# Kernel tuning notes

Measured on AMD Instinct MI355X. Metric: run time of the kernel, lower is better.

Reference implementation:

```python
import jax, jax.numpy as jnp
import numpy as np

D = 1024
H = 8
B, S = 4, 2048


def setup_inputs() -> dict:
    key = jax.random.key(0)
    ks = jax.random.split(key, 11)
    s = 0.02
    return {
        "Q": jax.random.normal(ks[0], (B, S, D), jnp.float32),
        "K": jax.random.normal(ks[1], (B, S, D), jnp.float32),
        "V": jax.random.normal(ks[2], (B, S, D), jnp.float32),
        "WQ": jax.random.normal(ks[3], (D, D), jnp.float32) * s,
        "bQ": jax.random.normal(ks[4], (D,), jnp.float32) * s,
        "WK": jax.random.normal(ks[5], (D, D), jnp.float32) * s,
        "bK": jax.random.normal(ks[6], (D,), jnp.float32) * s,
        "WV": jax.random.normal(ks[7], (D, D), jnp.float32) * s,
        "bV": jax.random.normal(ks[8], (D,), jnp.float32) * s,
        "Wl": jax.random.normal(ks[9], (D, D * H), jnp.float32) * s,
        "bl": jax.random.normal(ks[10], (D,), jnp.float32) * s,
    }


def reference(Q, K, V, WQ, bQ, WK, bK, WV, bV, Wl, bl):
    # SelfAttention (weights shared across all heads in the original module)
    q = Q @ WQ.T + bQ  # [B,S,D]
    k = K @ WK.T + bK
    v = V @ WV.T + bV
    scale = 1.0 / np.sqrt(D).astype(np.float32)
    scores = jnp.einsum('bqd,bkd->bqk', q, k) * scale  # [B,S,S]
    attn = jax.nn.softmax(scores, axis=-1)
    Z = jnp.einsum('bqk,bkd->bqd', attn, v)  # [B,S,D]
    # concat of H identical copies, then linear(D*H -> D)
    Zcat = jnp.tile(Z, (1, 1, H))  # [B,S,D*H]
    return Zcat @ Wl.T + bl
```

## Files before the change

kernel.cpp:

```cpp
#include <hip/hip_runtime.h>
#include <stdint.h>

#define DEV __device__ __forceinline__

typedef __attribute__((ext_vector_type(8))) unsigned short frag8;
typedef __attribute__((ext_vector_type(4))) float f32x4;
typedef __attribute__((ext_vector_type(8))) unsigned short ushort8;
typedef __attribute__((ext_vector_type(4))) unsigned short ushort4v;

DEV unsigned short f2bf(float f) {
  union { float f; unsigned u; } x; x.f = f;
  unsigned r = x.u + 0x7fffu + ((x.u >> 16) & 1u);
  return (unsigned short)(r >> 16);
}
DEV float bf2f(unsigned short b) {
  union { unsigned u; float f; } x; x.u = ((unsigned)b) << 16;
  return x.f;
}

DEV void gload_lds16(const void* g, void* l) {
  __builtin_amdgcn_global_load_lds((const __attribute__((address_space(1))) void*)g,
                                   (__attribute__((address_space(3))) void*)l, 16, 0, 0);
}

DEV void mfma_bf16(f32x4& c, frag8 a, frag8 b) {
  asm("v_mfma_f32_16x16x32_bf16 %0, %1, %2, %0" : "+v"(c) : "v"(a), "v"(b));
}

DEV void wait_vm0_barrier() {
  asm volatile("s_waitcnt vmcnt(0)" ::: "memory");
  __builtin_amdgcn_s_barrier();
  asm volatile("" ::: "memory");
  __builtin_amdgcn_sched_barrier(0);
}

template<int BIAS, int SCALEF, int MODE>
__global__ __launch_bounds__(256)
void gemm_bt(const unsigned short* __restrict__ A,
             const unsigned short* __restrict__ Bm,
             const float* __restrict__ bias0, const float* __restrict__ bias1,
             const float* __restrict__ bias2,
             void* __restrict__ Cv,
             int N, int K, float scale,
             long sA, long sB, long sC,
             int nx, int ny)
{
  __shared__ unsigned short lds[2][2][128 * 64];

  const int tid  = threadIdx.x;
  const int lane = tid & 63;
  const int wave = tid >> 6;
  const int wm   = wave >> 1;
  const int wn   = wave & 1;

  const unsigned nwg = gridDim.x;
  const unsigned orig = blockIdx.x;
  const unsigned qq = nwg >> 3, rr = nwg & 7;
  const unsigned xcd = orig & 7, jj = orig >> 3;
  const unsigned wg = (xcd < rr ? xcd * (qq + 1) : rr * (qq + 1) + (xcd - rr) * qq) + jj;
  const unsigned bx = wg % (unsigned)nx;
  const unsigned tt = wg / (unsigned)nx;
  const unsigned by = tt % (unsigned)ny;
  const unsigned bz = tt / (unsigned)ny;

  const int bm = (int)by * 128;
  const int bn = (int)bx * 128;

  A  += (size_t)bz * (size_t)sA;
  Bm += (size_t)bz * (size_t)sB;

  const int r8  = lane >> 3;
  const int l8  = lane & 7;
  const int swz = ((l8 ^ r8) << 4);
  const size_t Kb = (size_t)K * 2;

  const char* gA = (const char*)A  + (size_t)(bm + wave * 32 + r8) * Kb + swz;
  const char* gB = (const char*)Bm + (size_t)(bn + wave * 32 + r8) * Kb + swz;
  char* lA0 = (char*)&lds[0][0][0] + wave * 32 * 128;
  char* lB0 = (char*)&lds[0][1][0] + wave * 32 * 128;
  char* lA1 = (char*)&lds[1][0][0] + wave * 32 * 128;
  char* lB1 = (char*)&lds[1][1][0] + wave * 32 * 128;

  const int cr = lane & 15;
  const int kq = lane >> 4;
  const int base16 = ((kq ^ (cr & 7)) << 4);
  const char* rA0 = (const char*)&lds[0][0][0] + (wm * 64 + cr) * 128;
  const char* rB0 = (const char*)&lds[0][1][0] + (wn * 64 + cr) * 128;
  const char* rA1 = (const char*)&lds[1][0][0] + (wm * 64 + cr) * 128;
  const char* rB1 = (const char*)&lds[1][1][0] + (wn * 64 + cr) * 128;

  f32x4 acc[4][4];
  #pragma unroll
  for (int m = 0; m < 4; ++m)
    #pragma unroll
    for (int n = 0; n < 4; ++n)
      acc[m][n] = f32x4{0.f, 0.f, 0.f, 0.f};

  auto STAGE = [&](int t, char* la, char* lb) {
    const char* ga = gA + (size_t)t * 128;
    const char* gb = gB + (size_t)t * 128;
    gload_lds16(ga,               la);
    gload_lds16(gb,               lb);
    gload_lds16(ga +  8 * Kb,     la + 1024);
    gload_lds16(gb +  8 * Kb,     lb + 1024);
    gload_lds16(ga + 16 * Kb,     la + 2048);
    gload_lds16(gb + 16 * Kb,     lb + 2048);
    gload_lds16(ga + 24 * Kb,     la + 3072);
    gload_lds16(gb + 24 * Kb,     lb + 3072);
  };
  auto COMPUTE = [&](const char* ra, const char* rb) {
    #pragma unroll
    for (int kk = 0; kk < 2; ++kk) {
      const int off = base16 ^ (kk << 6);
      frag8 a[4], b[4];
      #pragma unroll
      for (int f = 0; f < 4; ++f) {
        a[f] = *(const frag8*)(ra + f * 2048 + off);
        b[f] = *(const frag8*)(rb + f * 2048 + off);
      }
      #pragma unroll
      for (int m = 0; m < 4; ++m)
        #pragma unroll
        for (int n = 0; n < 4; ++n)
          mfma_bf16(acc[m][n], a[m], b[n]);
    }
  };

  const int nk = K >> 6;
  STAGE(0, lA0, lB0);
  wait_vm0_barrier();
  for (int kt = 0; kt < nk; kt += 2) {
    STAGE(kt + 1, lA1, lB1);
    COMPUTE(rA0, rB0);
    wait_vm0_barrier();
    if (kt + 2 < nk) STAGE(kt + 2, lA0, lB0);
    COMPUTE(rA1, rB1);
    wait_vm0_barrier();
  }

  const float* bias = bias0;
  if constexpr (MODE == 2) bias = (bz == 0) ? bias0 : (bz == 1) ? bias1 : bias2;

  #pragma unroll
  for (int m = 0; m < 4; ++m) {
    const int gr0 = bm + wm * 64 + m * 16 + kq * 4;
    #pragma unroll
    for (int n = 0; n < 4; ++n) {
      const int gc = bn + wn * 64 + n * 16 + cr;
      float bb = 0.f;
      if constexpr (BIAS) bb = bias[gc];
      float v0 = acc[m][n][0], v1 = acc[m][n][1], v2 = acc[m][n][2], v3 = acc[m][n][3];
      if constexpr (SCALEF) { v0 *= scale; v1 *= scale; v2 *= scale; v3 *= scale; }
      v0 += bb; v1 += bb; v2 += bb; v3 += bb;
      if constexpr (MODE == 1) {
        float* C = (float*)Cv + (size_t)bz * (size_t)sC;
        C[(size_t)(gr0 + 0) * N + gc] = v0;
        C[(size_t)(gr0 + 1) * N + gc] = v1;
        C[(size_t)(gr0 + 2) * N + gc] = v2;
        C[(size_t)(gr0 + 3) * N + gc] = v3;
      } else if constexpr (MODE == 2) {
        if (bz == 2) {
          unsigned short* C = (unsigned short*)Cv + (size_t)2 * (size_t)sC;
          ushort4v u;
          u[0] = f2bf(v0); u[1] = f2bf(v1); u[2] = f2bf(v2); u[3] = f2bf(v3);
          *(ushort4v*)&C[((size_t)(gr0 >> 11) << 21) + (size_t)gc * 2048 + (gr0 & 2047)] = u;
        } else {
          unsigned short* C = (unsigned short*)Cv + (size_t)bz * (size_t)sC;
          C[(size_t)(gr0 + 0) * N + gc] = f2bf(v0);
          C[(size_t)(gr0 + 1) * N + gc] = f2bf(v1);
          C[(size_t)(gr0 + 2) * N + gc] = f2bf(v2);
          C[(size_t)(gr0 + 3) * N + gc] = f2bf(v3);
        }
      } else {
        unsigned short* C = (unsigned short*)Cv + (size_t)bz * (size_t)sC;
        C[(size_t)(gr0 + 0) * N + gc] = f2bf(v0);
        C[(size_t)(gr0 + 1) * N + gc] = f2bf(v1);
        C[(size_t)(gr0 + 2) * N + gc] = f2bf(v2);
        C[(size_t)(gr0 + 3) * N + gc] = f2bf(v3);
      }
    }
  }
}

__global__ __launch_bounds__(256)
void softmax_rows(unsigned short* __restrict__ P, int S)
{
  const int tid = threadIdx.x;
  unsigned short* pr = P + (size_t)blockIdx.x * S;

  ushort8 u = *(const ushort8*)(pr + tid * 8);
  float v[8];
  float mx = -1e30f;
  #pragma unroll
  for (int j = 0; j < 8; ++j) { v[j] = bf2f(u[j]); mx = fmaxf(mx, v[j]); }

  #pragma unroll
  for (int off = 32; off; off >>= 1) mx = fmaxf(mx, __shfl_xor(mx, off));

  __shared__ float red[8];
  const int wid = tid >> 6;
  if ((tid & 63) == 0) red[wid] = mx;
  __syncthreads();
  mx = fmaxf(fmaxf(red[0], red[1]), fmaxf(red[2], red[3]));

  float e[8], s = 0.f;
  #pragma unroll
  for (int j = 0; j < 8; ++j) { e[j] = __expf(v[j] - mx); s += e[j]; }
  #pragma unroll
  for (int off = 32; off; off >>= 1) s += __shfl_xor(s, off);
  if ((tid & 63) == 0) red[4 + wid] = s;
  __syncthreads();
  s = red[4] + red[5] + red[6] + red[7];

  const float inv = 1.f / s;
  ushort8 o;
  #pragma unroll
  for (int j = 0; j < 8; ++j) o[j] = f2bf(e[j] * inv);
  *(ushort8*)(pr + tid * 8) = o;
}

__global__ __launch_bounds__(256)
void cvt3_bf16(const float* __restrict__ s0, const float* __restrict__ s1,
               const float* __restrict__ s2, unsigned short* __restrict__ out,
               int n8each)
{
  const float* src = (blockIdx.y == 0) ? s0 : (blockIdx.y == 1) ? s1 : s2;
  unsigned short* dst = out + (size_t)blockIdx.y * ((size_t)n8each * 8);
  int i = blockIdx.x * blockDim.x + threadIdx.x;
  const int stride = gridDim.x * blockDim.x;
  for (; i < n8each; i += stride) {
    const float4* p = (const float4*)src + (size_t)i * 2;
    float4 a = p[0], b = p[1];
    ushort8 o;
    o[0] = f2bf(a.x); o[1] = f2bf(a.y); o[2] = f2bf(a.z); o[3] = f2bf(a.w);
    o[4] = f2bf(b.x); o[5] = f2bf(b.y); o[6] = f2bf(b.z); o[7] = f2bf(b.w);
    *((ushort8*)dst + i) = o;
  }
}

__global__ __launch_bounds__(256)
void weff_kernel(const float* __restrict__ Wl, unsigned short* __restrict__ out)
{
  const int idx = blockIdx.x * 256 + threadIdx.x;
  const int j = idx >> 8;
  const int d = (idx & 255) << 2;
  float4 s = make_float4(0.f, 0.f, 0.f, 0.f);
  #pragma unroll
  for (int h = 0; h < 8; ++h) {
    float4 w = *(const float4*)&Wl[(size_t)j * 8192 + h * 1024 + d];
    s.x += w.x; s.y += w.y; s.z += w.z; s.w += w.w;
  }
  ushort4v o;
  o[0] = f2bf(s.x); o[1] = f2bf(s.y); o[2] = f2bf(s.z); o[3] = f2bf(s.w);
  *(ushort4v*)&out[(size_t)j * 1024 + d] = o;
}

extern "C" void kernel_launch(void* const* d_in, const int* in_sizes, int n_in,
                              void* d_out, int out_size, void* d_ws, size_t ws_size,
                              hipStream_t stream)
{
  (void)in_sizes; (void)n_in; (void)out_size; (void)ws_size;

  const float* Q  = (const float*)d_in[0];
  const float* K  = (const float*)d_in[1];
  const float* V  = (const float*)d_in[2];
  const float* WQ = (const float*)d_in[3];
  const float* bQ = (const float*)d_in[4];
  const float* WK = (const float*)d_in[5];
  const float* bK = (const float*)d_in[6];
  const float* WV = (const float*)d_in[7];
  const float* bV = (const float*)d_in[8];
  const float* Wl = (const float*)d_in[9];
  const float* bl = (const float*)d_in[10];

  const size_t nX = (size_t)8192 * 1024;
  const size_t nW = (size_t)1024 * 1024;

  unsigned short* Qb  = (unsigned short*)d_ws;
  unsigned short* Vb  = Qb + 2 * nX;
  unsigned short* qb  = Vb + nX;
  unsigned short* vT  = qb + 2 * nX;
  unsigned short* Wqb = vT + nX;
  unsigned short* Wef = Wqb + 3 * nW;
  unsigned short* P   = Qb;
  unsigned short* kb  = qb + nX;
  unsigned short* Zb  = Vb;

  const int thr = 256;

  cvt3_bf16<<<dim3(1024, 3), thr, 0, stream>>>(Q, K, V, Qb, (int)(nX / 8));
  cvt3_bf16<<<dim3(512, 3),  thr, 0, stream>>>(WQ, WK, WV, Wqb, (int)(nW / 8));
  weff_kernel<<<1024, thr, 0, stream>>>(Wl, Wef);

  gemm_bt<1, 0, 2><<<1536, thr, 0, stream>>>(
      Qb, Wqb, bQ, bK, bV, qb, 1024, 1024, 1.f,
      (long)nX, (long)nW, (long)nX, 8, 64);
  gemm_bt<0, 1, 0><<<1024, thr, 0, stream>>>(
      qb, kb, nullptr, nullptr, nullptr, P, 2048, 1024, 0.03125f,
      (long)(2048 * 1024), (long)(2048 * 1024), (long)(2048 * 2048), 16, 16);
  softmax_rows<<<8192, thr, 0, stream>>>(P, 2048);
  gemm_bt<0, 0, 0><<<512, thr, 0, stream>>>(
      P, vT, nullptr, nullptr, nullptr, Zb, 1024, 2048, 1.f,
      (long)(2048 * 2048), (long)(1024 * 2048), (long)(2048 * 1024), 8, 16);
  gemm_bt<1, 0, 1><<<512, thr, 0, stream>>>(
      Zb, Wef, bl, nullptr, nullptr, d_out, 1024, 1024, 1.f,
      0, 0, 0, 8, 64);
}
```

Measured before the change: 212.8 us.

## Fuse softmax into score and PV GEMM epilogues; pipeline K loop with partial waits

```diff
diff --git a/kernel.cpp b/kernel.cpp
--- a/kernel.cpp
+++ b/kernel.cpp
@@ -27,19 +27,28 @@
   asm("v_mfma_f32_16x16x32_bf16 %0, %1, %2, %0" : "+v"(c) : "v"(a), "v"(b));
 }
 
+DEV void wait_vm8_barrier() {
+  asm volatile("s_waitcnt vmcnt(8)" ::: "memory");
+  __builtin_amdgcn_s_barrier();
+  __builtin_amdgcn_sched_barrier(0);
+}
 DEV void wait_vm0_barrier() {
   asm volatile("s_waitcnt vmcnt(0)" ::: "memory");
   __builtin_amdgcn_s_barrier();
-  asm volatile("" ::: "memory");
   __builtin_amdgcn_sched_barrier(0);
 }
-
-template<int BIAS, int SCALEF, int MODE>
+DEV void raw_barrier() {
+  __builtin_amdgcn_s_barrier();
+  __builtin_amdgcn_sched_barrier(0);
+}
+
+template<int BIAS, int MODE>
 __global__ __launch_bounds__(256)
 void gemm_bt(const unsigned short* __restrict__ A,
              const unsigned short* __restrict__ Bm,
              const float* __restrict__ bias0, const float* __restrict__ bias1,
              const float* __restrict__ bias2,
+             float* __restrict__ rowsum,
              void* __restrict__ Cv,
              int N, int K, float scale,
              long sA, long sB, long sC,
@@ -128,14 +137,16 @@
 
   const int nk = K >> 6;
   STAGE(0, lA0, lB0);
-  wait_vm0_barrier();
-  for (int kt = 0; kt < nk; kt += 2) {
-    STAGE(kt + 1, lA1, lB1);
-    COMPUTE(rA0, rB0);
-    wait_vm0_barrier();
-    if (kt + 2 < nk) STAGE(kt + 2, lA0, lB0);
-    COMPUTE(rA1, rB1);
-    wait_vm0_barrier();
+  for (int t = 0; t < nk; ++t) {
+    const bool odd = t & 1;
+    if (t + 1 < nk) {
+      STAGE(t + 1, odd ? lA0 : lA1, odd ? lB0 : lB1);
+      wait_vm8_barrier();
+    } else {
+      wait_vm0_barrier();
+    }
+    COMPUTE(odd ? rA1 : rA0, odd ? rB1 : rB0);
+    raw_barrier();
   }
 
   const float* bias = bias0;
@@ -144,13 +155,18 @@
   #pragma unroll
   for (int m = 0; m < 4; ++m) {
     const int gr0 = bm + wm * 64 + m * 16 + kq * 4;
+    float psum[4] = {0.f, 0.f, 0.f, 0.f};
+    float inv0 = 1.f, inv1 = 1.f, inv2 = 1.f, inv3 = 1.f;
+    if constexpr (MODE == 4) {
+      const float4 rs = *(const float4*)&bias0[(size_t)bz * 2048 + gr0];
+      inv0 = 1.f / rs.x; inv1 = 1.f / rs.y; inv2 = 1.f / rs.z; inv3 = 1.f / rs.w;
+    }
     #pragma unroll
     for (int n = 0; n < 4; ++n) {
       const int gc = bn + wn * 64 + n * 16 + cr;
       float bb = 0.f;
       if constexpr (BIAS) bb = bias[gc];
       float v0 = acc[m][n][0], v1 = acc[m][n][1], v2 = acc[m][n][2], v3 = acc[m][n][3];
-      if constexpr (SCALEF) { v0 *= scale; v1 *= scale; v2 *= scale; v3 *= scale; }
       v0 += bb; v1 += bb; v2 += bb; v3 += bb;
       if constexpr (MODE == 1) {
         float* C = (float*)Cv + (size_t)bz * (size_t)sC;
@@ -158,6 +174,24 @@
         C[(size_t)(gr0 + 1) * N + gc] = v1;
         C[(size_t)(gr0 + 2) * N + gc] = v2;
         C[(size_t)(gr0 + 3) * N + gc] = v3;
+      } else if constexpr (MODE == 3) {
+        unsigned short* C = (unsigned short*)Cv + (size_t)bz * (size_t)sC;
+        unsigned short e0 = f2bf(__expf(v0 * scale));
+        unsigned short e1 = f2bf(__expf(v1 * scale));
+        unsigned short e2 = f2bf(__expf(v2 * scale));
+        unsigned short e3 = f2bf(__expf(v3 * scale));
+        C[(size_t)(gr0 + 0) * N + gc] = e0;
+        C[(size_t)(gr0 + 1) * N + gc] = e1;
+        C[(size_t)(gr0 + 2) * N + gc] = e2;
+        C[(size_t)(gr0 + 3) * N + gc] = e3;
+        psum[0] += bf2f(e0); psum[1] += bf2f(e1);
+        psum[2] += bf2f(e2); psum[3] += bf2f(e3);
+      } else if constexpr (MODE == 4) {
+        unsigned short* C = (unsigned short*)Cv + (size_t)bz * (size_t)sC;
+        C[(size_t)(gr0 + 0) * N + gc] = f2bf(v0 * inv0);
+        C[(size_t)(gr0 + 1) * N + gc] = f2bf(v1 * inv1);
+        C[(size_t)(gr0 + 2) * N + gc] = f2bf(v2 * inv2);
+        C[(size_t)(gr0 + 3) * N + gc] = f2bf(v3 * inv3);
       } else if constexpr (MODE == 2) {
         if (bz == 2) {
           unsigned short* C = (unsigned short*)Cv + (size_t)2 * (size_t)sC;
@@ -179,44 +213,18 @@
         C[(size_t)(gr0 + 3) * N + gc] = f2bf(v3);
       }
     }
+    if constexpr (MODE == 3) {
+      #pragma unroll
+      for (int j = 0; j < 4; ++j) {
+        float p = psum[j];
+        p += __shfl_xor(p, 1);
+        p += __shfl_xor(p, 2);
+        p += __shfl_xor(p, 4);
+        p += __shfl_xor(p, 8);
+        if (cr == 0) atomicAdd(&rowsum[(size_t)bz * 2048 + gr0 + j], p);
+      }
+    }
   }
-}
-
-__global__ __launch_bounds__(256)
-void softmax_rows(unsigned short* __restrict__ P, int S)
-{
-  const int tid = threadIdx.x;
-  unsigned short* pr = P + (size_t)blockIdx.x * S;
-
-  ushort8 u = *(const ushort8*)(pr + tid * 8);
-  float v[8];
-  float mx = -1e30f;
-  #pragma unroll
-  for (int j = 0; j < 8; ++j) { v[j] = bf2f(u[j]); mx = fmaxf(mx, v[j]); }
-
-  #pragma unroll
-  for (int off = 32; off; off >>= 1) mx = fmaxf(mx, __shfl_xor(mx, off));
-
-  __shared__ float red[8];
-  const int wid = tid >> 6;
-  if ((tid & 63) == 0) red[wid] = mx;
-  __syncthreads();
-  mx = fmaxf(fmaxf(red[0], red[1]), fmaxf(red[2], red[3]));
-
-  float e[8], s = 0.f;
-  #pragma unroll
-  for (int j = 0; j < 8; ++j) { e[j] = __expf(v[j] - mx); s += e[j]; }
-  #pragma unroll
-  for (int off = 32; off; off >>= 1) s += __shfl_xor(s, off);
-  if ((tid & 63) == 0) red[4 + wid] = s;
-  __syncthreads();
-  s = red[4] + red[5] + red[6] + red[7];
-
-  const float inv = 1.f / s;
-  ushort8 o;
-  #pragma unroll
-  for (int j = 0; j < 8; ++j) o[j] = f2bf(e[j] * inv);
-  *(ushort8*)(pr + tid * 8) = o;
 }
 
 __global__ __launch_bounds__(256)
@@ -255,6 +263,13 @@
   *(ushort4v*)&out[(size_t)j * 1024 + d] = o;
 }
 
+__global__ __launch_bounds__(256)
+void zero_f32(float* __restrict__ p, int n)
+{
+  const int i = blockIdx.x * 256 + threadIdx.x;
+  if (i < n) p[i] = 0.f;
+}
+
 extern "C" void kernel_launch(void* const* d_in, const int* in_sizes, int n_in,
                               void* d_out, int out_size, void* d_ws, size_t ws_size,
                               hipStream_t stream)
@@ -282,6 +297,7 @@
   unsigned short* vT  = qb + 2 * nX;
   unsigned short* Wqb = vT + nX;
   unsigned short* Wef = Wqb + 3 * nW;
+  float*          rowsum = (float*)(Wef + nW);
   unsigned short* P   = Qb;
   unsigned short* kb  = qb + nX;
   unsigned short* Zb  = Vb;
@@ -291,18 +307,18 @@
   cvt3_bf16<<<dim3(1024, 3), thr, 0, stream>>>(Q, K, V, Qb, (int)(nX / 8));
   cvt3_bf16<<<dim3(512, 3),  thr, 0, stream>>>(WQ, WK, WV, Wqb, (int)(nW / 8));
   weff_kernel<<<1024, thr, 0, stream>>>(Wl, Wef);
-
-  gemm_bt<1, 0, 2><<<1536, thr, 0, stream>>>(
-      Qb, Wqb, bQ, bK, bV, qb, 1024, 1024, 1.f,
+  zero_f32<<<32, thr, 0, stream>>>(rowsum, 8192);
+
+  gemm_bt<1, 2><<<1536, thr, 0, stream>>>(
+      Qb, Wqb, bQ, bK, bV, nullptr, qb, 1024, 1024, 1.f,
       (long)nX, (long)nW, (long)nX, 8, 64);
-  gemm_bt<0, 1, 0><<<1024, thr, 0, stream>>>(
-      qb, kb, nullptr, nullptr, nullptr, P, 2048, 1024, 0.03125f,
+  gemm_bt<0, 3><<<1024, thr, 0, stream>>>(
+      qb, kb, nullptr, nullptr, nullptr, rowsum, P, 2048, 1024, 0.03125f,
       (long)(2048 * 1024), (long)(2048 * 1024), (long)(2048 * 2048), 16, 16);
-  softmax_rows<<<8192, thr, 0, stream>>>(P, 2048);
-  gemm_bt<0, 0, 0><<<512, thr, 0, stream>>>(
-      P, vT, nullptr, nullptr, nullptr, Zb, 1024, 2048, 1.f,
+  gemm_bt<0, 4><<<512, thr, 0, stream>>>(
+      P, vT, rowsum, nullptr, nullptr, nullptr, Zb, 1024, 2048, 1.f,
       (long)(2048 * 2048), (long)(1024 * 2048), (long)(2048 * 1024), 8, 16);
-  gemm_bt<1, 0, 1><<<512, thr, 0, stream>>>(
-      Zb, Wef, bl, nullptr, nullptr, d_out, 1024, 1024, 1.f,
+  gemm_bt<1, 1><<<512, thr, 0, stream>>>(
+      Zb, Wef, bl, nullptr, nullptr, nullptr, d_out, 1024, 1024, 1.f,
       0, 0, 0, 8, 64);
 }
```

Measured after the change: 217.5 us. 2.2% more time.
